# Kernel optimization log

Hardware: AMD Instinct MI355X
Metric: run time of the kernel (lower is better)

## Reference

```python
import jax, jax.numpy as jnp
import numpy as np

DIM = 1024
D_STATE = 16

def setup_inputs() -> dict:
    key = jax.random.key(0)
    kx, ka, kd = jax.random.split(key, 3)
    x = jax.random.normal(kx, (4, 8192, DIM), dtype=jnp.float32)
    A = jax.random.normal(ka, (DIM, D_STATE), dtype=jnp.float32)
    D = jax.random.normal(kd, (D_STATE, DIM), dtype=jnp.float32)
    return {"x": x, "A": A, "D": D}

def reference(x, A, D):
    # x: [B, N, C]; A: [C, S]; D: [S, C]
    x_state = jnp.einsum('bnc,cs->bns', x, A)        # [B, N, S]
    x_state = jnp.cumsum(x_state, axis=1)            # prefix sum over sequence
    out = jnp.einsum('bns,sc->bnc', x_state, D)      # [B, N, C]
    return out
```

## Files before the change

kernel.cpp:

```cpp
#include <hip/hip_runtime.h>

#define DIM   1024
#define DST   16
#define NSEQ  8192
#define NB    4

typedef __attribute__((ext_vector_type(8))) short  short8;
typedef __attribute__((ext_vector_type(4))) float  floatx4;

__device__ inline unsigned bf16_rne_bits(float f) {
    unsigned u = __float_as_uint(f);
    return (u + 0x7fffu + ((u >> 16) & 1u)) >> 16;
}

#define KP 1032

__global__ __launch_bounds__(256) void k1_mfma(const float* __restrict__ x,
                                               const float* __restrict__ A,
                                               float* __restrict__ T) {
    __shared__ unsigned short abHi[DST * KP];
    __shared__ unsigned short abLo[DST * KP];
    const int t  = threadIdx.x;
    const int b  = blockIdx.x >> 7;
    const int n0 = (blockIdx.x & 127) * 64;

    for (int i = t; i < DIM * DST; i += 256) {
        const int s = i & 15, k = i >> 4;
        const float a = A[i];
        const unsigned hb = bf16_rne_bits(a);
        const float ah = __uint_as_float(hb << 16);
        const unsigned lb = bf16_rne_bits(a - ah);
        abHi[s * KP + k] = (unsigned short)hb;
        abLo[s * KP + k] = (unsigned short)lb;
    }
    __syncthreads();

    const int wave = t >> 6;
    const int lane = t & 63;
    const int m    = lane & 15;
    const int q    = lane >> 4;

    const int row = n0 + wave * 16 + m;
    const float* xp = x + ((long)(b * NSEQ + row)) * DIM + q * 8;
    const unsigned short* bh = &abHi[m * KP + q * 8];
    const unsigned short* bl = &abLo[m * KP + q * 8];

    floatx4 acc = {0.f, 0.f, 0.f, 0.f};

    float4 c0 = *(const float4*)(xp);
    float4 c1 = *(const float4*)(xp + 4);

    for (int step = 0; step < 32; ++step) {
        const int ns = (step + 1) & 31;
        const float4 p0 = *(const float4*)(xp + ns * 32);
        const float4 p1 = *(const float4*)(xp + ns * 32 + 4);

        short8 ahi, alo;
        const float cf[8] = {c0.x, c0.y, c0.z, c0.w, c1.x, c1.y, c1.z, c1.w};
        #pragma unroll
        for (int j = 0; j < 8; ++j) {
            const unsigned hb = bf16_rne_bits(cf[j]);
            const float fh = __uint_as_float(hb << 16);
            const unsigned lb = bf16_rne_bits(cf[j] - fh);
            ahi[j] = (short)hb;
            alo[j] = (short)lb;
        }
        const short8 bhi = *(const short8*)(bh + step * 32);
        const short8 blo = *(const short8*)(bl + step * 32);

        acc = __builtin_amdgcn_mfma_f32_16x16x32_bf16(ahi, bhi, acc, 0, 0, 0);
        acc = __builtin_amdgcn_mfma_f32_16x16x32_bf16(alo, bhi, acc, 0, 0, 0);
        acc = __builtin_amdgcn_mfma_f32_16x16x32_bf16(ahi, blo, acc, 0, 0, 0);

        c0 = p0; c1 = p1;
    }

    float* tp = &T[((long)(b * DST + m)) * NSEQ + n0 + wave * 16 + q * 4];
    *(floatx4*)tp = acc;
}

__global__ __launch_bounds__(256) void k2_scan(float* __restrict__ T) {
    __shared__ float wsum[4];
    const int t = threadIdx.x;
    const int b = blockIdx.x >> 4;
    const int s = blockIdx.x & 15;
    float* row = T + ((long)(b * DST + s)) * NSEQ;
    const int base = t * 32;

    float v[32];
    #pragma unroll
    for (int j = 0; j < 8; ++j) {
        const float4 f = *(const float4*)&row[base + 4 * j];
        v[4 * j + 0] = f.x; v[4 * j + 1] = f.y;
        v[4 * j + 2] = f.z; v[4 * j + 3] = f.w;
    }
    float run = 0.f;
    #pragma unroll
    for (int i = 0; i < 32; ++i) { run += v[i]; v[i] = run; }

    const int lane = t & 63;
    float sc = run;
    #pragma unroll
    for (int off = 1; off < 64; off <<= 1) {
        const float u = __shfl_up(sc, off, 64);
        if (lane >= off) sc += u;
    }
    const int w = t >> 6;
    if (lane == 63) wsum[w] = sc;
    __syncthreads();

    float woff = 0.f;
    #pragma unroll
    for (int i = 0; i < 4; ++i) woff += (i < w) ? wsum[i] : 0.f;
    const float excl = woff + sc - run;

    #pragma unroll
    for (int j = 0; j < 8; ++j) {
        const float4 f = make_float4(v[4 * j + 0] + excl, v[4 * j + 1] + excl,
                                     v[4 * j + 2] + excl, v[4 * j + 3] + excl);
        *(float4*)&row[base + 4 * j] = f;
    }
}

#define K3_W 64

__global__ __launch_bounds__(256) void k3_out(const float* __restrict__ T,
                                              const float* __restrict__ D,
                                              float* __restrict__ out) {
    __shared__ float sp[K3_W * 20];
    const int t  = threadIdx.x;
    const int b  = blockIdx.x >> 7;
    const int n0 = (blockIdx.x & 127) * K3_W;

    #pragma unroll
    for (int j = 0; j < 4; ++j) {
        const int idx = j * 256 + t;
        const int ss  = idx >> 6;
        const int nn  = idx & 63;
        sp[nn * 20 + ss] = T[((long)(b * DST + ss)) * NSEQ + n0 + nn];
    }

    float4 dreg[16];
    #pragma unroll
    for (int ss = 0; ss < 16; ++ss)
        dreg[ss] = *(const float4*)&D[ss * DIM + 4 * t];

    __syncthreads();

    float* ob = out + ((long)(b * NSEQ + n0)) * DIM + 4 * t;
    for (int r = 0; r < K3_W; ++r) {
        const float4 s0 = *(const float4*)&sp[r * 20 + 0];
        const float4 s1 = *(const float4*)&sp[r * 20 + 4];
        const float4 s2 = *(const float4*)&sp[r * 20 + 8];
        const float4 s3 = *(const float4*)&sp[r * 20 + 12];
        const float sv[16] = {s0.x, s0.y, s0.z, s0.w, s1.x, s1.y, s1.z, s1.w,
                              s2.x, s2.y, s2.z, s2.w, s3.x, s3.y, s3.z, s3.w};
        float4 o = make_float4(0.f, 0.f, 0.f, 0.f);
        #pragma unroll
        for (int ss = 0; ss < 16; ++ss) {
            o.x += sv[ss] * dreg[ss].x;
            o.y += sv[ss] * dreg[ss].y;
            o.z += sv[ss] * dreg[ss].z;
            o.w += sv[ss] * dreg[ss].w;
        }
        *(float4*)(ob + (long)r * DIM) = o;
    }
}

extern "C" void kernel_launch(void* const* d_in, const int* in_sizes, int n_in,
                              void* d_out, int out_size, void* d_ws, size_t ws_size,
                              hipStream_t stream) {
    const float* x = (const float*)d_in[0];
    const float* A = (const float*)d_in[1];
    const float* D = (const float*)d_in[2];
    float* out = (float*)d_out;
    float* T   = (float*)d_ws;

    k1_mfma<<<dim3(NB * 128), dim3(256), 0, stream>>>(x, A, T);
    k2_scan<<<dim3(NB * DST), dim3(256), 0, stream>>>(T);
    k3_out <<<dim3(NB * 128), dim3(256), 0, stream>>>(T, D, out);
}
```

Before: 288.7 us.

## Fuse scan into projection kernels via chunked local scan and carry totals

```diff
diff --git a/kernel.cpp b/kernel.cpp
--- a/kernel.cpp
+++ b/kernel.cpp
@@ -4,6 +4,7 @@
 #define DST   16
 #define NSEQ  8192
 #define NB    4
+#define NCH   128
 
 typedef __attribute__((ext_vector_type(8))) short  short8;
 typedef __attribute__((ext_vector_type(4))) float  floatx4;
@@ -15,23 +16,33 @@
 
 #define KP 1032
 
-__global__ __launch_bounds__(256) void k1_mfma(const float* __restrict__ x,
-                                               const float* __restrict__ A,
-                                               float* __restrict__ T) {
+__global__ __launch_bounds__(256, 2) void kA(const float* __restrict__ x,
+                                             const float* __restrict__ A,
+                                             float* __restrict__ Tl,
+                                             float* __restrict__ ct) {
     __shared__ unsigned short abHi[DST * KP];
     __shared__ unsigned short abLo[DST * KP];
-    const int t  = threadIdx.x;
-    const int b  = blockIdx.x >> 7;
-    const int n0 = (blockIdx.x & 127) * 64;
+    __shared__ float wtot[4][16];
+    const int t     = threadIdx.x;
+    const int b     = blockIdx.x >> 7;
+    const int chunk = blockIdx.x & 127;
+    const int n0    = chunk * 64;
 
-    for (int i = t; i < DIM * DST; i += 256) {
-        const int s = i & 15, k = i >> 4;
-        const float a = A[i];
-        const unsigned hb = bf16_rne_bits(a);
-        const float ah = __uint_as_float(hb << 16);
-        const unsigned lb = bf16_rne_bits(a - ah);
-        abHi[s * KP + k] = (unsigned short)hb;
-        abLo[s * KP + k] = (unsigned short)lb;
+    #pragma unroll
+    for (int j = 0; j < 16; ++j) {
+        const int f  = (j * 256 + t) * 4;
+        const int k  = f >> 4;
+        const int s0 = f & 15;
+        const float4 a4 = *(const float4*)&A[f];
+        const float av[4] = {a4.x, a4.y, a4.z, a4.w};
+        #pragma unroll
+        for (int i = 0; i < 4; ++i) {
+            const unsigned hb = bf16_rne_bits(av[i]);
+            const float ah = __uint_as_float(hb << 16);
+            const unsigned lb = bf16_rne_bits(av[i] - ah);
+            abHi[(s0 + i) * KP + k] = (unsigned short)hb;
+            abLo[(s0 + i) * KP + k] = (unsigned short)lb;
+        }
     }
     __syncthreads();
 
@@ -40,20 +51,27 @@
     const int m    = lane & 15;
     const int q    = lane >> 4;
 
-    const int row = n0 + wave * 16 + m;
-    const float* xp = x + ((long)(b * NSEQ + row)) * DIM + q * 8;
+    const float* xp = x + ((long)(b * NSEQ + n0 + wave * 16 + m)) * DIM + q * 8;
     const unsigned short* bh = &abHi[m * KP + q * 8];
     const unsigned short* bl = &abLo[m * KP + q * 8];
 
     floatx4 acc = {0.f, 0.f, 0.f, 0.f};
 
-    float4 c0 = *(const float4*)(xp);
-    float4 c1 = *(const float4*)(xp + 4);
+    float4 pf[4][2];
+    #pragma unroll
+    for (int i = 0; i < 4; ++i) {
+        pf[i][0] = *(const float4*)(xp + i * 32);
+        pf[i][1] = *(const float4*)(xp + i * 32 + 4);
+    }
 
+    #pragma unroll 4
     for (int step = 0; step < 32; ++step) {
-        const int ns = (step + 1) & 31;
-        const float4 p0 = *(const float4*)(xp + ns * 32);
-        const float4 p1 = *(const float4*)(xp + ns * 32 + 4);
+        const int slot = step & 3;
+        const float4 c0 = pf[slot][0];
+        const float4 c1 = pf[slot][1];
+        const int ns = (step + 4) & 31;
+        pf[slot][0] = *(const float4*)(xp + ns * 32);
+        pf[slot][1] = *(const float4*)(xp + ns * 32 + 4);
 
         short8 ahi, alo;
         const float cf[8] = {c0.x, c0.y, c0.z, c0.w, c1.x, c1.y, c1.z, c1.w};
@@ -71,73 +89,50 @@
         acc = __builtin_amdgcn_mfma_f32_16x16x32_bf16(ahi, bhi, acc, 0, 0, 0);
         acc = __builtin_amdgcn_mfma_f32_16x16x32_bf16(alo, bhi, acc, 0, 0, 0);
         acc = __builtin_amdgcn_mfma_f32_16x16x32_bf16(ahi, blo, acc, 0, 0, 0);
-
-        c0 = p0; c1 = p1;
     }
 
-    float* tp = &T[((long)(b * DST + m)) * NSEQ + n0 + wave * 16 + q * 4];
-    *(floatx4*)tp = acc;
-}
-
-__global__ __launch_bounds__(256) void k2_scan(float* __restrict__ T) {
-    __shared__ float wsum[4];
-    const int t = threadIdx.x;
-    const int b = blockIdx.x >> 4;
-    const int s = blockIdx.x & 15;
-    float* row = T + ((long)(b * DST + s)) * NSEQ;
-    const int base = t * 32;
-
-    float v[32];
-    #pragma unroll
-    for (int j = 0; j < 8; ++j) {
-        const float4 f = *(const float4*)&row[base + 4 * j];
-        v[4 * j + 0] = f.x; v[4 * j + 1] = f.y;
-        v[4 * j + 2] = f.z; v[4 * j + 3] = f.w;
+    acc[1] += acc[0]; acc[2] += acc[1]; acc[3] += acc[2];
+    const float g = acc[3];
+    float v = g;
+    {
+        const float u1 = __shfl_up(v, 16, 64); if (lane >= 16) v += u1;
+        const float u2 = __shfl_up(v, 32, 64); if (lane >= 32) v += u2;
     }
-    float run = 0.f;
-    #pragma unroll
-    for (int i = 0; i < 32; ++i) { run += v[i]; v[i] = run; }
-
-    const int lane = t & 63;
-    float sc = run;
-    #pragma unroll
-    for (int off = 1; off < 64; off <<= 1) {
-        const float u = __shfl_up(sc, off, 64);
-        if (lane >= off) sc += u;
-    }
-    const int w = t >> 6;
-    if (lane == 63) wsum[w] = sc;
+    const float exclq = v - g;
+    if (lane >= 48) wtot[wave][m] = v;
     __syncthreads();
 
     float woff = 0.f;
     #pragma unroll
-    for (int i = 0; i < 4; ++i) woff += (i < w) ? wsum[i] : 0.f;
-    const float excl = woff + sc - run;
+    for (int w = 0; w < 4; ++w) woff += (w < wave) ? wtot[w][m] : 0.f;
+    const float add = exclq + woff;
+    acc[0] += add; acc[1] += add; acc[2] += add; acc[3] += add;
 
-    #pragma unroll
-    for (int j = 0; j < 8; ++j) {
-        const float4 f = make_float4(v[4 * j + 0] + excl, v[4 * j + 1] + excl,
-                                     v[4 * j + 2] + excl, v[4 * j + 3] + excl);
-        *(float4*)&row[base + 4 * j] = f;
+    if (t < 16) {
+        const float tot = wtot[0][t] + wtot[1][t] + wtot[2][t] + wtot[3][t];
+        ct[((long)(b * DST + t)) * NCH + chunk] = tot;
     }
+
+    float* tp = &Tl[(((long)(b * NCH + chunk)) * DST + m) * 64 + wave * 16 + q * 4];
+    *(floatx4*)tp = acc;
 }
 
-#define K3_W 64
+__global__ __launch_bounds__(256) void kB(const float* __restrict__ Tl,
+                                          const float* __restrict__ ct,
+                                          const float* __restrict__ D,
+                                          float* __restrict__ out) {
+    __shared__ float sp[64 * 20];
+    __shared__ float pe[16];
+    const int t     = threadIdx.x;
+    const int b     = blockIdx.x >> 7;
+    const int chunk = blockIdx.x & 127;
+    const int n0    = chunk * 64;
 
-__global__ __launch_bounds__(256) void k3_out(const float* __restrict__ T,
-                                              const float* __restrict__ D,
-                                              float* __restrict__ out) {
-    __shared__ float sp[K3_W * 20];
-    const int t  = threadIdx.x;
-    const int b  = blockIdx.x >> 7;
-    const int n0 = (blockIdx.x & 127) * K3_W;
-
-    #pragma unroll
-    for (int j = 0; j < 4; ++j) {
-        const int idx = j * 256 + t;
-        const int ss  = idx >> 6;
-        const int nn  = idx & 63;
-        sp[nn * 20 + ss] = T[((long)(b * DST + ss)) * NSEQ + n0 + nn];
+    if (t < 16) {
+        const float* p = &ct[((long)(b * DST + t)) * NCH];
+        float s = 0.f;
+        for (int c = 0; c < chunk; ++c) s += p[c];
+        pe[t] = s;
     }
 
     float4 dreg[16];
@@ -147,8 +142,20 @@
 
     __syncthreads();
 
+    {
+        const int s4 = (4 * t) >> 6;
+        const int nn = (4 * t) & 63;
+        const float4 v = *(const float4*)&Tl[(((long)(b * NCH + chunk)) * DST + s4) * 64 + nn];
+        const float p = pe[s4];
+        sp[(nn + 0) * 20 + s4] = v.x + p;
+        sp[(nn + 1) * 20 + s4] = v.y + p;
+        sp[(nn + 2) * 20 + s4] = v.z + p;
+        sp[(nn + 3) * 20 + s4] = v.w + p;
+    }
+    __syncthreads();
+
     float* ob = out + ((long)(b * NSEQ + n0)) * DIM + 4 * t;
-    for (int r = 0; r < K3_W; ++r) {
+    for (int r = 0; r < 64; ++r) {
         const float4 s0 = *(const float4*)&sp[r * 20 + 0];
         const float4 s1 = *(const float4*)&sp[r * 20 + 4];
         const float4 s2 = *(const float4*)&sp[r * 20 + 8];
@@ -174,9 +181,9 @@
     const float* A = (const float*)d_in[1];
     const float* D = (const float*)d_in[2];
     float* out = (float*)d_out;
-    float* T   = (float*)d_ws;
+    float* Tl  = (float*)d_ws;
+    float* ct  = Tl + (long)NB * NCH * DST * 64;
 
-    k1_mfma<<<dim3(NB * 128), dim3(256), 0, stream>>>(x, A, T);
-    k2_scan<<<dim3(NB * DST), dim3(256), 0, stream>>>(T);
-    k3_out <<<dim3(NB * 128), dim3(256), 0, stream>>>(T, D, out);
+    kA<<<dim3(NB * NCH), dim3(256), 0, stream>>>(x, A, Tl, ct);
+    kB<<<dim3(NB * NCH), dim3(256), 0, stream>>>(Tl, ct, D, out);
 }
```

After: 278.7 us. 1.04x faster.
